# Kernel tuning notes

Hardware: AMD Instinct MI355X
Metric: run time of the kernel (lower is better)

The kernel has to match this reference:

```python
import jax, jax.numpy as jnp
import numpy as np

G, U, M = 4096, 50, 20          # groups, max users/group, max behaviors/user
D, S = 64, 64                   # emb dim (user==item), similarity dim
USER_NUM, ITEM_NUM = 100000, 100000
FACTOR = 0.5


def setup_inputs() -> dict:
    key = jax.random.key(0)
    k = jax.random.split(key, 7)
    group_user = jax.random.randint(k[0], (G, U), 0, USER_NUM, dtype=jnp.int32)
    behavior_ids = jax.random.randint(k[1], (G, U, M), 0, ITEM_NUM, dtype=jnp.int32)
    behavior_counts = jax.random.uniform(k[2], (G, U, M), dtype=jnp.float32)
    target_user = jax.random.randint(k[3], (G,), 0, USER_NUM, dtype=jnp.int32)
    similarity_vec = jax.random.normal(k[4], (USER_NUM, S), dtype=jnp.float32)
    # nn.Embedding(padding_idx=0): row 0 is zeros
    user_emb_w = jax.random.normal(k[5], (USER_NUM, D), dtype=jnp.float32).at[0].set(0.0)
    item_emb_w = jax.random.normal(k[6], (ITEM_NUM, D), dtype=jnp.float32).at[0].set(0.0)
    return {
        "group_user": group_user,
        "behavior_ids": behavior_ids,
        "behavior_counts": behavior_counts,
        "target_user": target_user,
        "similarity_vec": similarity_vec,
        "user_emb_w": user_emb_w,
        "item_emb_w": item_emb_w,
    }


def reference(group_user, behavior_ids, behavior_counts, target_user,
              similarity_vec, user_emb_w, item_emb_w) -> jnp.ndarray:
    # Per-user weighted sum of behavior item embeddings: [G,U,D]
    beh_emb = item_emb_w[behavior_ids]                         # [G,U,M,D] (big gather)
    user_behavior = jnp.sum(beh_emb * behavior_counts[..., None], axis=2)  # [G,U,D]
    # Personalize with user embedding (elementwise product)
    users_emb = user_emb_w[group_user]                         # [G,U,D]
    personalized = user_behavior * users_emb                   # [G,U,D]
    # Similarity weighting: factor * (target_sim . other_sim) per user
    others_sim = similarity_vec[group_user]                    # [G,U,S]
    target_sim = similarity_vec[target_user]                   # [G,S]
    sim = FACTOR * jnp.einsum('gs,gus->gu', target_sim, others_sim)  # [G,U]
    # Weighted sum over users in group -> group embedding [G,D]
    return jnp.sum(personalized * sim[..., None], axis=1)
```

## Files before the change

### kernel.cpp

```cpp
#include <hip/hip_runtime.h>
#include <hip/hip_bf16.h>


constexpr int G = 4096;
constexpr int U = 50;
constexpr int M = 20;
constexpr int D = 64;
constexpr int S = 64;
constexpr float FACTOR = 0.5f;

__global__ __launch_bounds__(256) void group_embedding_kernel(
    const int*   __restrict__ group_user,
    const int*   __restrict__ behavior_ids,
    const float* __restrict__ behavior_counts,
    const int*   __restrict__ target_user,
    const float* __restrict__ similarity_vec,
    const float* __restrict__ user_emb_w,
    const float* __restrict__ item_emb_w,
    float*       __restrict__ out)
{
    const int g    = blockIdx.x;
    const int tid  = threadIdx.x;
    const int wave = tid >> 6;
    const int lane = tid & 63;

    const int   tgt  = target_user[g];
    const float tsim = similarity_vec[(size_t)tgt * S + lane];

    float acc = 0.0f;

    #pragma unroll 2
    for (int u = wave; u < U; u += 4) {
        const int gu = group_user[g * U + u];

        float p = tsim * similarity_vec[(size_t)gu * S + lane];
        #pragma unroll
        for (int off = 32; off > 0; off >>= 1)
            p += __shfl_xor(p, off);
        const float sim = FACTOR * p;

        const int bbase = (g * U + u) * M;
        int   ids [M];
        float cnts[M];
        #pragma unroll
        for (int m = 0; m < M; ++m) {
            ids [m] = behavior_ids   [bbase + m];
            cnts[m] = behavior_counts[bbase + m];
        }
        float ub = 0.0f;
        #pragma unroll
        for (int m = 0; m < M; ++m) {
            ub = fmaf(item_emb_w[(size_t)ids[m] * D + lane], cnts[m], ub);
        }

        const float ue = user_emb_w[(size_t)gu * D + lane];
        acc = fmaf(ub * ue, sim, acc);
    }

    __shared__ float red[4][D];
    red[wave][lane] = acc;
    __syncthreads();
    if (wave == 0) {
        out[(size_t)g * D + lane] =
            red[0][lane] + red[1][lane] + red[2][lane] + red[3][lane];
    }
}

extern "C" void kernel_launch(void* const* d_in, const int* in_sizes, int n_in,
                              void* d_out, int out_size, void* d_ws, size_t ws_size,
                              hipStream_t stream) {
    const int*   group_user      = (const int*)  d_in[0];
    const int*   behavior_ids    = (const int*)  d_in[1];
    const float* behavior_counts = (const float*)d_in[2];
    const int*   target_user     = (const int*)  d_in[3];
    const float* similarity_vec  = (const float*)d_in[4];
    const float* user_emb_w      = (const float*)d_in[5];
    const float* item_emb_w      = (const float*)d_in[6];
    float*       out             = (float*)d_out;

    group_embedding_kernel<<<G, 256, 0, stream>>>(
        group_user, behavior_ids, behavior_counts, target_user,
        similarity_vec, user_emb_w, item_emb_w, out);
}
```

Baseline: 257.2 us.

## Stage behavior ids in LDS and gather four users per wave with float4

Each block first loads the group's behavior ids, counts and user ids into shared memory, padding the user count to 64 with id 0. Each wave then processes four users at once, with 16 lanes per user reading float4 slices of the embedding and similarity rows. Partial sums are reduced with shuffles and LDS. The goal is more memory-level parallelism, wider loads and coalesced index reads. In exchange it adds 14 padded users whose loads hit the zero row, plus an extra barrier and more LDS use.

Result: slower. 264.0 us (+2.6%).

```diff
diff --git a/kernel.cpp b/kernel.cpp
--- a/kernel.cpp
+++ b/kernel.cpp
@@ -7,6 +7,7 @@
 constexpr int M = 20;
 constexpr int D = 64;
 constexpr int S = 64;
+constexpr int UPAD = 64;
 constexpr float FACTOR = 0.5f;
 
 __global__ __launch_bounds__(256) void group_embedding_kernel(
@@ -23,46 +24,78 @@
     const int tid  = threadIdx.x;
     const int wave = tid >> 6;
     const int lane = tid & 63;
+    const int uu   = lane >> 4;
+    const int q    = lane & 15;
 
-    const int   tgt  = target_user[g];
-    const float tsim = similarity_vec[(size_t)tgt * S + lane];
+    __shared__ int    gu_lds[UPAD];
+    __shared__ int    ids_lds[UPAD * M];
+    __shared__ float  cnt_lds[UPAD * M];
+    __shared__ float4 red[4][16];
 
-    float acc = 0.0f;
+    for (int i = tid; i < UPAD * M; i += 256) {
+        const bool v = (i < U * M);
+        ids_lds[i] = v ? behavior_ids  [(size_t)g * U * M + i] : 0;
+        cnt_lds[i] = v ? behavior_counts[(size_t)g * U * M + i] : 0.0f;
+    }
+    if (tid < UPAD) gu_lds[tid] = (tid < U) ? group_user[g * U + tid] : 0;
+    __syncthreads();
 
-    #pragma unroll 2
-    for (int u = wave; u < U; u += 4) {
-        const int gu = group_user[g * U + u];
+    const int tgt = target_user[g];
+    const float4 tsim = *(const float4*)(similarity_vec + (size_t)tgt * S + 4 * q);
 
-        float p = tsim * similarity_vec[(size_t)gu * S + lane];
-        #pragma unroll
-        for (int off = 32; off > 0; off >>= 1)
-            p += __shfl_xor(p, off);
+    float4 acc = {0.f, 0.f, 0.f, 0.f};
+
+    #pragma unroll 1
+    for (int iter = 0; iter < UPAD / 16; ++iter) {
+        const int u  = iter * 16 + wave * 4 + uu;
+        const int gu = gu_lds[u];
+
+        const float4 sv = *(const float4*)(similarity_vec + (size_t)gu * S + 4 * q);
+        float p = tsim.x * sv.x + tsim.y * sv.y + tsim.z * sv.z + tsim.w * sv.w;
+        p += __shfl_xor(p, 1);
+        p += __shfl_xor(p, 2);
+        p += __shfl_xor(p, 4);
+        p += __shfl_xor(p, 8);
         const float sim = FACTOR * p;
 
-        const int bbase = (g * U + u) * M;
-        int   ids [M];
-        float cnts[M];
+        const float4 ue = *(const float4*)(user_emb_w + (size_t)gu * D + 4 * q);
+
+        float4 ub = {0.f, 0.f, 0.f, 0.f};
         #pragma unroll
         for (int m = 0; m < M; ++m) {
-            ids [m] = behavior_ids   [bbase + m];
-            cnts[m] = behavior_counts[bbase + m];
-        }
-        float ub = 0.0f;
-        #pragma unroll
-        for (int m = 0; m < M; ++m) {
-            ub = fmaf(item_emb_w[(size_t)ids[m] * D + lane], cnts[m], ub);
+            const int   id = ids_lds[u * M + m];
+            const float c  = cnt_lds[u * M + m];
+            const float4 it = *(const float4*)(item_emb_w + (size_t)id * D + 4 * q);
+            ub.x = fmaf(it.x, c, ub.x);
+            ub.y = fmaf(it.y, c, ub.y);
+            ub.z = fmaf(it.z, c, ub.z);
+            ub.w = fmaf(it.w, c, ub.w);
         }
 
-        const float ue = user_emb_w[(size_t)gu * D + lane];
-        acc = fmaf(ub * ue, sim, acc);
+        acc.x = fmaf(ub.x * ue.x, sim, acc.x);
+        acc.y = fmaf(ub.y * ue.y, sim, acc.y);
+        acc.z = fmaf(ub.z * ue.z, sim, acc.z);
+        acc.w = fmaf(ub.w * ue.w, sim, acc.w);
     }
 
-    __shared__ float red[4][D];
-    red[wave][lane] = acc;
+    #pragma unroll
+    for (int off = 16; off < 64; off <<= 1) {
+        acc.x += __shfl_xor(acc.x, off);
+        acc.y += __shfl_xor(acc.y, off);
+        acc.z += __shfl_xor(acc.z, off);
+        acc.w += __shfl_xor(acc.w, off);
+    }
+    if (uu == 0) red[wave][q] = acc;
     __syncthreads();
-    if (wave == 0) {
-        out[(size_t)g * D + lane] =
-            red[0][lane] + red[1][lane] + red[2][lane] + red[3][lane];
+
+    if (wave == 0 && uu == 0) {
+        const float4 r0 = red[0][q], r1 = red[1][q], r2 = red[2][q], r3 = red[3][q];
+        float4 o;
+        o.x = r0.x + r1.x + r2.x + r3.x;
+        o.y = r0.y + r1.y + r2.y + r3.y;
+        o.z = r0.z + r1.z + r2.z + r3.z;
+        o.w = r0.w + r1.w + r2.w + r3.w;
+        *(float4*)(out + (size_t)g * D + 4 * q) = o;
     }
 }
 
```
